# Kernel tuning notes

Measured on AMD Instinct MI355X. Metric: run time of the kernel, lower is better.

## Reference

```python
import jax, jax.numpy as jnp
import numpy as np

N = 100000
E = 200000
SD = 128   # structural_dim
CD = 768   # chemical_dim


def _linear_params(key, fan_in, fan_out):
    kw, kb = jax.random.split(key)
    bound = 1.0 / np.sqrt(fan_in)
    W = jax.random.uniform(kw, (fan_in, fan_out), jnp.float32, -bound, bound)
    b = jax.random.uniform(kb, (fan_out,), jnp.float32, -bound, bound)
    return W, b


def setup_inputs() -> dict:
    key = jax.random.key(0)
    ks = jax.random.split(key, 12)
    z = jax.random.normal(ks[0], (N, SD), jnp.float32)
    chemistry = jax.random.normal(ks[1], (N, CD), jnp.float32)
    edge = jax.random.randint(ks[2], (E, 2), 0, N, jnp.int64)
    smiles_mask = jax.random.randint(ks[3], (N,), 0, 2, jnp.int32)
    # structural_mlp: SD -> SD//2 -> 1
    sw1, sb1 = _linear_params(ks[4], SD, SD // 2)
    sw2, sb2 = _linear_params(ks[5], SD // 2, 1)
    # chemical_mlp: CD -> CD//4 -> 1
    cw1, cb1 = _linear_params(ks[6], CD, CD // 4)
    cw2, cb2 = _linear_params(ks[7], CD // 4, 1)
    # combined_mlp: SD+CD -> SD -> 1
    mw1, mb1 = _linear_params(ks[8], SD + CD, SD)
    mw2, mb2 = _linear_params(ks[9], SD, 1)
    path_weights = jnp.ones((3,), jnp.float32) / 3.0
    return dict(z=z, chemistry=chemistry, edge=edge, smiles_mask=smiles_mask,
                sw1=sw1, sb1=sb1, sw2=sw2, sb2=sb2,
                cw1=cw1, cb1=cb1, cw2=cw2, cb2=cb2,
                mw1=mw1, mb1=mb1, mw2=mw2, mb2=mb2,
                path_weights=path_weights)


def reference(z, chemistry, edge, smiles_mask,
              sw1, sb1, sw2, sb2,
              cw1, cb1, cw2, cb2,
              mw1, mb1, mw2, mb2,
              path_weights):
    src, dst = edge[:, 0], edge[:, 1]
    # per-edge gathers + elementwise products
    structural_prod = z[src] * z[dst]                    # [E, SD]
    chemical_prod = chemistry[src] * chemistry[dst]      # [E, CD]
    # three small MLPs (dropout is identity in eval mode)
    score_structural = (jax.nn.relu(structural_prod @ sw1 + sb1) @ sw2 + sb2)[:, 0]
    score_chemical = (jax.nn.relu(chemical_prod @ cw1 + cb1) @ cw2 + cb2)[:, 0]
    combined_prod = jnp.concatenate([structural_prod, chemical_prod], axis=-1)  # [E, SD+CD]
    score_combined = (jax.nn.relu(combined_prod @ mw1 + mb1) @ mw2 + mb2)[:, 0]
    # fixed learned path weights (use_gating=False)
    w = jax.nn.softmax(path_weights)
    scores = w[0] * score_structural + w[1] * score_chemical + w[2] * score_combined
    # fall back to structural-only score where chemistry is missing on either end
    mask = smiles_mask.astype(z.dtype)
    both_valid = mask[src] * mask[dst]
    return jnp.where(both_valid > 0.5, scores, score_structural)  # [E]
```

## Files before the change

### kernel.cpp

```cpp
#include <hip/hip_runtime.h>


typedef float  f32x4  __attribute__((ext_vector_type(4)));
typedef __bf16 bf16x8 __attribute__((ext_vector_type(8)));
typedef unsigned short u16x4 __attribute__((ext_vector_type(4)));

static_assert(sizeof(bf16x8) == 16, "bf16x8 must be 16B");
static_assert(sizeof(f32x4) == 16, "f32x4 must be 16B");

#define N_NODES 100000
#define E_EDGES 200000
#define KSTEPS  28
#define NOUT    384
#define PTOT    (KSTEPS * NOUT * 32)

#define WS_WHI   0
#define WS_WLO   688128
#define WS_B1    1376256
#define WS_W2    1377792
#define WS_CONST 1379328

__device__ __forceinline__ unsigned short f2bf(float f) {
  unsigned int x = __float_as_uint(f);
  unsigned int r = (x + 0x7FFFu + ((x >> 16) & 1u)) >> 16;
  return (unsigned short)r;
}
__device__ __forceinline__ float bf2f(unsigned short u) {
  return __uint_as_float(((unsigned int)u) << 16);
}

__global__ __launch_bounds__(256) void prep_kernel(
    const float* __restrict__ sw1, const float* __restrict__ sb1,
    const float* __restrict__ sw2, const float* __restrict__ sb2,
    const float* __restrict__ cw1, const float* __restrict__ cb1,
    const float* __restrict__ cw2, const float* __restrict__ cb2,
    const float* __restrict__ mw1, const float* __restrict__ mb1,
    const float* __restrict__ mw2, const float* __restrict__ mb2,
    const float* __restrict__ pw,  const int* __restrict__ edge_i32,
    unsigned short* __restrict__ whi, unsigned short* __restrict__ wlo,
    float* __restrict__ b1cat, float* __restrict__ w2cat,
    float* __restrict__ consts)
{
  const int idx = blockIdx.x * 256 + threadIdx.x;
  if (idx < PTOT) {
    const int p  = idx / (NOUT * 32);
    const int r  = idx % (NOUT * 32);
    const int n  = r >> 5;
    const int kk = r & 31;
    const int k  = p * 32 + kk;
    float v;
    if (n < 64)       v = (k < 128)  ? sw1[k * 64 + n] : 0.0f;
    else if (n < 256) v = (k >= 128) ? cw1[(size_t)(k - 128) * 192 + (n - 64)] : 0.0f;
    else              v = mw1[(size_t)k * 128 + (n - 256)];
    const unsigned short hi = f2bf(v);
    const unsigned short lo = f2bf(v - bf2f(hi));
    whi[idx] = hi;
    wlo[idx] = lo;
  } else if (idx < PTOT + NOUT) {
    const int j = idx - PTOT;
    float b, w;
    if (j < 64)       { b = sb1[j];       w = sw2[j]; }
    else if (j < 256) { b = cb1[j - 64];  w = cw2[j - 64]; }
    else              { b = mb1[j - 256]; w = mw2[j - 256]; }
    b1cat[j] = b;
    w2cat[j] = w;
  } else if (idx == PTOT + NOUT) {
    const float p0 = pw[0], p1 = pw[1], p2 = pw[2];
    const float mx = fmaxf(p0, fmaxf(p1, p2));
    const float e0 = __expf(p0 - mx), e1 = __expf(p1 - mx), e2 = __expf(p2 - mx);
    const float inv = 1.0f / (e0 + e1 + e2);
    const float w0 = e0 * inv, w1 = e1 * inv, w2v = e2 * inv;
    consts[0] = w0; consts[1] = w1; consts[2] = w2v;
    consts[3] = w0 * sb2[0] + w1 * cb2[0] + w2v * mb2[0];
    consts[4] = sb2[0];
    unsigned o = 0;
    for (int i = 0; i < 64; ++i) o |= (unsigned)edge_i32[2 * i + 1];
    consts[5] = (o == 0u) ? 1.0f : 0.0f;
  }
}

__global__ __launch_bounds__(256, 2) void decoder_main(
    const float* __restrict__ z, const float* __restrict__ chem,
    const int* __restrict__ edge, const int* __restrict__ mask,
    const unsigned short* __restrict__ whi, const unsigned short* __restrict__ wlo,
    const float* __restrict__ b1cat, const float* __restrict__ w2cat,
    const float* __restrict__ consts, float* __restrict__ out)
{
  __shared__ unsigned short Ah[2][64][40];
  __shared__ unsigned short Al[2][64][40];
  __shared__ int   srcL[64];
  __shared__ int   dstL[64];
  __shared__ float validL[64];
  __shared__ float scoreL[64];

  const int tid  = threadIdx.x;
  const int lane = tid & 63;
  const int wv   = tid >> 6;
  const int li   = lane & 15;
  const int q    = lane >> 4;
  const int m0   = blockIdx.x << 6;

  if (tid < 64) {
    scoreL[tid] = 0.0f;
    const int e = m0 + tid;
    int s_, d_;
    if (consts[5] > 0.5f) { s_ = edge[4 * e]; d_ = edge[4 * e + 2]; }
    else                  { s_ = edge[2 * e]; d_ = edge[2 * e + 1]; }
    srcL[tid] = s_;
    dstL[tid] = d_;
    validL[tid] = (mask[s_] != 0 && mask[d_] != 0) ? 1.0f : 0.0f;
  }
  __syncthreads();

  const int mA = tid >> 3;
  const int mB = 32 + mA;
  const int kc = (tid & 7) << 2;
  const float* zsA = z + (size_t)srcL[mA] * 128 + kc;
  const float* zdA = z + (size_t)dstL[mA] * 128 + kc;
  const float* zsB = z + (size_t)srcL[mB] * 128 + kc;
  const float* zdB = z + (size_t)dstL[mB] * 128 + kc;
  const float* csA = chem + (size_t)srcL[mA] * 768 + kc;
  const float* cdA = chem + (size_t)dstL[mA] * 768 + kc;
  const float* csB = chem + (size_t)srcL[mB] * 768 + kc;
  const float* cdB = chem + (size_t)dstL[mB] * 768 + kc;

  auto split_store = [&](int buf, int m, f32x4 p) {
    u16x4 h, l;
#pragma unroll
    for (int j = 0; j < 4; ++j) {
      const unsigned short hj = f2bf(p[j]);
      h[j] = hj;
      l[j] = f2bf(p[j] - bf2f(hj));
    }
    *(u16x4*)&Ah[buf][m][kc] = h;
    *(u16x4*)&Al[buf][m][kc] = l;
  };

  {
    const f32x4 a0 = *(const f32x4*)zsA;
    const f32x4 b0 = *(const f32x4*)zdA;
    const f32x4 a1 = *(const f32x4*)zsB;
    const f32x4 b1 = *(const f32x4*)zdB;
    split_store(0, mA, a0 * b0);
    split_store(0, mB, a1 * b1);
  }
  __syncthreads();

  f32x4 acc[4][6];
#pragma unroll
  for (int mt = 0; mt < 4; ++mt)
#pragma unroll
    for (int i = 0; i < 6; ++i)
      acc[mt][i] = (f32x4){0.f, 0.f, 0.f, 0.f};

  for (int s = 0; s < KSTEPS; ++s) {
    const int buf = s & 1;

    bf16x8 afh[4], afl[4];
#pragma unroll
    for (int mt = 0; mt < 4; ++mt) {
      afh[mt] = *(const bf16x8*)&Ah[buf][mt * 16 + li][q * 8];
      afl[mt] = *(const bf16x8*)&Al[buf][mt * 16 + li][q * 8];
    }

    bf16x8 bfh[6], bfl[6];
    bool act[6];
#pragma unroll
    for (int i = 0; i < 6; ++i) {
      const int ti = wv + 4 * i;
      const int path = (ti < 4) ? 0 : (ti < 16 ? 1 : 2);
      act[i] = (path == 0) ? (s < 4) : (path == 1) ? (s >= 4) : true;
      if (act[i]) {
        const size_t off = (size_t)s * (NOUT * 32) + (size_t)(ti * 16 + li) * 32 + q * 8;
        bfh[i] = *(const bf16x8*)(whi + off);
        bfl[i] = *(const bf16x8*)(wlo + off);
      }
    }

    f32x4 ga, gb, gc, gd;
    if (s + 1 < KSTEPS) {
      const int k0 = (s + 1) * 32;
      if (k0 < 128) {
        ga = *(const f32x4*)(zsA + k0); gb = *(const f32x4*)(zdA + k0);
        gc = *(const f32x4*)(zsB + k0); gd = *(const f32x4*)(zdB + k0);
      } else {
        const int ko = k0 - 128;
        ga = *(const f32x4*)(csA + ko); gb = *(const f32x4*)(cdA + ko);
        gc = *(const f32x4*)(csB + ko); gd = *(const f32x4*)(cdB + ko);
      }
    }

#pragma unroll
    for (int i = 0; i < 6; ++i) {
      if (act[i]) {
#pragma unroll
        for (int mt = 0; mt < 4; ++mt) {
          acc[mt][i] = __builtin_amdgcn_mfma_f32_16x16x32_bf16(afh[mt], bfh[i], acc[mt][i], 0, 0, 0);
          acc[mt][i] = __builtin_amdgcn_mfma_f32_16x16x32_bf16(afh[mt], bfl[i], acc[mt][i], 0, 0, 0);
          acc[mt][i] = __builtin_amdgcn_mfma_f32_16x16x32_bf16(afl[mt], bfh[i], acc[mt][i], 0, 0, 0);
        }
      }
    }

    if (s + 1 < KSTEPS) {
      const int nbuf = buf ^ 1;
      split_store(nbuf, mA, ga * gb);
      split_store(nbuf, mB, gc * gd);
    }
    __syncthreads();
  }

  float part[4][4];
#pragma unroll
  for (int mt = 0; mt < 4; ++mt)
#pragma unroll
    for (int r = 0; r < 4; ++r) part[mt][r] = 0.f;

  const float w0c = consts[0], w1c = consts[1], w2c = consts[2];
#pragma unroll
  for (int i = 0; i < 6; ++i) {
    const int ti = wv + 4 * i;
    const int path = (ti < 4) ? 0 : (ti < 16 ? 1 : 2);
    const int col = ti * 16 + li;
    const float b1 = b1cat[col];
    const float w2 = w2cat[col];
    const float wp  = (path == 0) ? w0c : (path == 1) ? w1c : w2c;
    const float p0f = (path == 0) ? 1.0f : 0.0f;
#pragma unroll
    for (int mt = 0; mt < 4; ++mt) {
#pragma unroll
      for (int r = 0; r < 4; ++r) {
        const float valid = validL[mt * 16 + q * 4 + r];
        const float a = p0f + valid * (wp - p0f);
        float v = acc[mt][i][r] + b1;
        v = fmaxf(v, 0.0f);
        part[mt][r] += a * v * w2;
      }
    }
  }

#pragma unroll
  for (int mt = 0; mt < 4; ++mt) {
#pragma unroll
    for (int r = 0; r < 4; ++r) {
      float v = part[mt][r];
      v += __shfl_xor(v, 1);
      v += __shfl_xor(v, 2);
      v += __shfl_xor(v, 4);
      v += __shfl_xor(v, 8);
      if (li == 0) atomicAdd(&scoreL[mt * 16 + q * 4 + r], v);
    }
  }
  __syncthreads();

  if (tid < 64) {
    const float valid = validL[tid];
    const float cadd = consts[4] + valid * (consts[3] - consts[4]);
    out[m0 + tid] = scoreL[tid] + cadd;
  }
}

extern "C" void kernel_launch(void* const* d_in, const int* in_sizes, int n_in,
                              void* d_out, int out_size, void* d_ws, size_t ws_size,
                              hipStream_t stream)
{
  const float* z    = (const float*)d_in[0];
  const float* chem = (const float*)d_in[1];
  const int*   edge = (const int*)d_in[2];
  const int*   mask = (const int*)d_in[3];
  const float* sw1  = (const float*)d_in[4];
  const float* sb1  = (const float*)d_in[5];
  const float* sw2  = (const float*)d_in[6];
  const float* sb2  = (const float*)d_in[7];
  const float* cw1  = (const float*)d_in[8];
  const float* cb1  = (const float*)d_in[9];
  const float* cw2  = (const float*)d_in[10];
  const float* cb2  = (const float*)d_in[11];
  const float* mw1  = (const float*)d_in[12];
  const float* mb1  = (const float*)d_in[13];
  const float* mw2  = (const float*)d_in[14];
  const float* mb2  = (const float*)d_in[15];
  const float* pw   = (const float*)d_in[16];

  char* ws = (char*)d_ws;
  unsigned short* whi = (unsigned short*)(ws + WS_WHI);
  unsigned short* wlo = (unsigned short*)(ws + WS_WLO);
  float* b1cat  = (float*)(ws + WS_B1);
  float* w2cat  = (float*)(ws + WS_W2);
  float* consts = (float*)(ws + WS_CONST);

  const int prep_tasks  = PTOT + NOUT + 64;
  const int prep_blocks = (prep_tasks + 255) / 256;
  prep_kernel<<<prep_blocks, 256, 0, stream>>>(
      sw1, sb1, sw2, sb2, cw1, cb1, cw2, cb2, mw1, mb1, mw2, mb2, pw, edge,
      whi, wlo, b1cat, w2cat, consts);

  decoder_main<<<E_EDGES / 64, 256, 0, stream>>>(
      z, chem, edge, mask, whi, wlo, b1cat, w2cat, consts, (float*)d_out);
}
```

Baseline: 761.5 us.

## Split K loop into structural and chemical phases to cut accumulator registers

The single 28-step loop with runtime per-tile activity checks is split into two loops: a 4-step structural phase and a 24-step chemical phase. The structural path's accumulators are reduced into shared scores and released before the chemical-only accumulators are allocated, so fewer accumulator registers are live at once. Launch bounds are raised from 2 to 3 blocks per SM to use that lower register pressure. The bf16 split now uses native __bf16 casts instead of hand-written rounding. Risks are register spills if three blocks do not fit, and an extra round of LDS atomics for the structural scores.

Measured after the change: 803.6 us. +5.5%, slower.

```diff
diff --git a/kernel.cpp b/kernel.cpp
--- a/kernel.cpp
+++ b/kernel.cpp
@@ -3,10 +3,7 @@
 
 typedef float  f32x4  __attribute__((ext_vector_type(4)));
 typedef __bf16 bf16x8 __attribute__((ext_vector_type(8)));
-typedef unsigned short u16x4 __attribute__((ext_vector_type(4)));
-
-static_assert(sizeof(bf16x8) == 16, "bf16x8 must be 16B");
-static_assert(sizeof(f32x4) == 16, "f32x4 must be 16B");
+typedef __bf16 bf16x4 __attribute__((ext_vector_type(4)));
 
 #define N_NODES 100000
 #define E_EDGES 200000
@@ -79,7 +76,12 @@
   }
 }
 
-__global__ __launch_bounds__(256, 2) void decoder_main(
+#define MFMA3(A, AH, AL, BH, BL)                                          \
+  A = __builtin_amdgcn_mfma_f32_16x16x32_bf16(AH, BH, A, 0, 0, 0);        \
+  A = __builtin_amdgcn_mfma_f32_16x16x32_bf16(AH, BL, A, 0, 0, 0);        \
+  A = __builtin_amdgcn_mfma_f32_16x16x32_bf16(AL, BH, A, 0, 0, 0);
+
+__global__ __launch_bounds__(256, 3) void decoder_main(
     const float* __restrict__ z, const float* __restrict__ chem,
     const int* __restrict__ edge, const int* __restrict__ mask,
     const unsigned short* __restrict__ whi, const unsigned short* __restrict__ wlo,
@@ -125,15 +127,16 @@
   const float* cdB = chem + (size_t)dstL[mB] * 768 + kc;
 
   auto split_store = [&](int buf, int m, f32x4 p) {
-    u16x4 h, l;
+    bf16x4 h, l;
 #pragma unroll
     for (int j = 0; j < 4; ++j) {
-      const unsigned short hj = f2bf(p[j]);
-      h[j] = hj;
-      l[j] = f2bf(p[j] - bf2f(hj));
-    }
-    *(u16x4*)&Ah[buf][m][kc] = h;
-    *(u16x4*)&Al[buf][m][kc] = l;
+      const float pj = p[j];
+      const __bf16 hb = (__bf16)pj;
+      h[j] = hb;
+      l[j] = (__bf16)(pj - (float)hb);
+    }
+    *(bf16x4*)&Ah[buf][m][kc] = h;
+    *(bf16x4*)&Al[buf][m][kc] = l;
   };
 
   {
@@ -146,109 +149,180 @@
   }
   __syncthreads();
 
-  f32x4 acc[4][6];
-#pragma unroll
-  for (int mt = 0; mt < 4; ++mt)
-#pragma unroll
-    for (int i = 0; i < 6; ++i)
-      acc[mt][i] = (f32x4){0.f, 0.f, 0.f, 0.f};
-
-  for (int s = 0; s < KSTEPS; ++s) {
+  const int colS  = ((wv)      * 16 + li) * 32 + q * 8;
+  const int colC0 = ((16 + wv) * 16 + li) * 32 + q * 8;
+  const int colC1 = ((20 + wv) * 16 + li) * 32 + q * 8;
+  const int colH0 = ((4 + wv)  * 16 + li) * 32 + q * 8;
+  const int colH1 = ((8 + wv)  * 16 + li) * 32 + q * 8;
+  const int colH2 = ((12 + wv) * 16 + li) * 32 + q * 8;
+
+  const float w0c = consts[0], w1c = consts[1], w2c = consts[2];
+
+  f32x4 accS[4], accC0[4], accC1[4];
+#pragma unroll
+  for (int mt = 0; mt < 4; ++mt) {
+    accS[mt] = (f32x4){0.f, 0.f, 0.f, 0.f};
+    accC0[mt] = (f32x4){0.f, 0.f, 0.f, 0.f};
+    accC1[mt] = (f32x4){0.f, 0.f, 0.f, 0.f};
+  }
+
+  for (int s = 0; s < 4; ++s) {
     const int buf = s & 1;
-
     bf16x8 afh[4], afl[4];
 #pragma unroll
     for (int mt = 0; mt < 4; ++mt) {
       afh[mt] = *(const bf16x8*)&Ah[buf][mt * 16 + li][q * 8];
       afl[mt] = *(const bf16x8*)&Al[buf][mt * 16 + li][q * 8];
     }
-
-    bf16x8 bfh[6], bfl[6];
-    bool act[6];
-#pragma unroll
-    for (int i = 0; i < 6; ++i) {
-      const int ti = wv + 4 * i;
-      const int path = (ti < 4) ? 0 : (ti < 16 ? 1 : 2);
-      act[i] = (path == 0) ? (s < 4) : (path == 1) ? (s >= 4) : true;
-      if (act[i]) {
-        const size_t off = (size_t)s * (NOUT * 32) + (size_t)(ti * 16 + li) * 32 + q * 8;
-        bfh[i] = *(const bf16x8*)(whi + off);
-        bfl[i] = *(const bf16x8*)(wlo + off);
-      }
-    }
+    const unsigned short* wph = whi + (size_t)s * (NOUT * 32);
+    const unsigned short* wpl = wlo + (size_t)s * (NOUT * 32);
+    const bf16x8 bSh  = *(const bf16x8*)(wph + colS);
+    const bf16x8 bSl  = *(const bf16x8*)(wpl + colS);
+    const bf16x8 bC0h = *(const bf16x8*)(wph + colC0);
+    const bf16x8 bC0l = *(const bf16x8*)(wpl + colC0);
+    const bf16x8 bC1h = *(const bf16x8*)(wph + colC1);
+    const bf16x8 bC1l = *(const bf16x8*)(wpl + colC1);
 
     f32x4 ga, gb, gc, gd;
-    if (s + 1 < KSTEPS) {
+    if (s < 3) {
       const int k0 = (s + 1) * 32;
-      if (k0 < 128) {
-        ga = *(const f32x4*)(zsA + k0); gb = *(const f32x4*)(zdA + k0);
-        gc = *(const f32x4*)(zsB + k0); gd = *(const f32x4*)(zdB + k0);
-      } else {
-        const int ko = k0 - 128;
-        ga = *(const f32x4*)(csA + ko); gb = *(const f32x4*)(cdA + ko);
-        gc = *(const f32x4*)(csB + ko); gd = *(const f32x4*)(cdB + ko);
-      }
-    }
-
-#pragma unroll
-    for (int i = 0; i < 6; ++i) {
-      if (act[i]) {
-#pragma unroll
-        for (int mt = 0; mt < 4; ++mt) {
-          acc[mt][i] = __builtin_amdgcn_mfma_f32_16x16x32_bf16(afh[mt], bfh[i], acc[mt][i], 0, 0, 0);
-          acc[mt][i] = __builtin_amdgcn_mfma_f32_16x16x32_bf16(afh[mt], bfl[i], acc[mt][i], 0, 0, 0);
-          acc[mt][i] = __builtin_amdgcn_mfma_f32_16x16x32_bf16(afl[mt], bfh[i], acc[mt][i], 0, 0, 0);
-        }
-      }
-    }
-
-    if (s + 1 < KSTEPS) {
-      const int nbuf = buf ^ 1;
-      split_store(nbuf, mA, ga * gb);
-      split_store(nbuf, mB, gc * gd);
-    }
+      ga = *(const f32x4*)(zsA + k0); gb = *(const f32x4*)(zdA + k0);
+      gc = *(const f32x4*)(zsB + k0); gd = *(const f32x4*)(zdB + k0);
+    } else {
+      ga = *(const f32x4*)csA; gb = *(const f32x4*)cdA;
+      gc = *(const f32x4*)csB; gd = *(const f32x4*)cdB;
+    }
+
+#pragma unroll
+    for (int mt = 0; mt < 4; ++mt) {
+      MFMA3(accS[mt],  afh[mt], afl[mt], bSh,  bSl);
+      MFMA3(accC0[mt], afh[mt], afl[mt], bC0h, bC0l);
+      MFMA3(accC1[mt], afh[mt], afl[mt], bC1h, bC1l);
+    }
+
+    const int nb = buf ^ 1;
+    split_store(nb, mA, ga * gb);
+    split_store(nb, mB, gc * gd);
     __syncthreads();
   }
 
-  float part[4][4];
-#pragma unroll
-  for (int mt = 0; mt < 4; ++mt)
-#pragma unroll
-    for (int r = 0; r < 4; ++r) part[mt][r] = 0.f;
-
-  const float w0c = consts[0], w1c = consts[1], w2c = consts[2];
-#pragma unroll
-  for (int i = 0; i < 6; ++i) {
-    const int ti = wv + 4 * i;
-    const int path = (ti < 4) ? 0 : (ti < 16 ? 1 : 2);
-    const int col = ti * 16 + li;
+  {
+    const int col = wv * 16 + li;
     const float b1 = b1cat[col];
     const float w2 = w2cat[col];
-    const float wp  = (path == 0) ? w0c : (path == 1) ? w1c : w2c;
-    const float p0f = (path == 0) ? 1.0f : 0.0f;
 #pragma unroll
     for (int mt = 0; mt < 4; ++mt) {
 #pragma unroll
       for (int r = 0; r < 4; ++r) {
         const float valid = validL[mt * 16 + q * 4 + r];
-        const float a = p0f + valid * (wp - p0f);
-        float v = acc[mt][i][r] + b1;
-        v = fmaxf(v, 0.0f);
-        part[mt][r] += a * v * w2;
+        const float a = 1.0f + valid * (w0c - 1.0f);
+        float v = fmaxf(accS[mt][r] + b1, 0.0f);
+        v = a * v * w2;
+        v += __shfl_xor(v, 1);
+        v += __shfl_xor(v, 2);
+        v += __shfl_xor(v, 4);
+        v += __shfl_xor(v, 8);
+        if (li == 0) atomicAdd(&scoreL[mt * 16 + q * 4 + r], v);
       }
     }
   }
 
+  f32x4 accH0[4], accH1[4], accH2[4];
 #pragma unroll
   for (int mt = 0; mt < 4; ++mt) {
-#pragma unroll
-    for (int r = 0; r < 4; ++r) {
-      float v = part[mt][r];
-      v += __shfl_xor(v, 1);
-      v += __shfl_xor(v, 2);
-      v += __shfl_xor(v, 4);
-      v += __shfl_xor(v, 8);
-      if (li == 0) atomicAdd(&scoreL[mt * 16 + q * 4 + r], v);
+    accH0[mt] = (f32x4){0.f, 0.f, 0.f, 0.f};
+    accH1[mt] = (f32x4){0.f, 0.f, 0.f, 0.f};
+    accH2[mt] = (f32x4){0.f, 0.f, 0.f, 0.f};
+  }
+
+  for (int s = 4; s < KSTEPS; ++s) {
+    const int buf = s & 1;
+    bf16x8 afh[4], afl[4];
+#pragma unroll
+    for (int mt = 0; mt < 4; ++mt) {
+      afh[mt] = *(const bf16x8*)&Ah[buf][mt * 16 + li][q * 8];
+      afl[mt] = *(const bf16x8*)&Al[buf][mt * 16 + li][q * 8];
+    }
+    const unsigned short* wph = whi + (size_t)s * (NOUT * 32);
+    const unsigned short* wpl = wlo + (size_t)s * (NOUT * 32);
+    const bf16x8 bC0h = *(const bf16x8*)(wph + colC0);
+    const bf16x8 bC0l = *(const bf16x8*)(wpl + colC0);
+    const bf16x8 bC1h = *(const bf16x8*)(wph + colC1);
+    const bf16x8 bC1l = *(const bf16x8*)(wpl + colC1);
+    const bf16x8 bH0h = *(const bf16x8*)(wph + colH0);
+    const bf16x8 bH0l = *(const bf16x8*)(wpl + colH0);
+    const bf16x8 bH1h = *(const bf16x8*)(wph + colH1);
+    const bf16x8 bH1l = *(const bf16x8*)(wpl + colH1);
+    const bf16x8 bH2h = *(const bf16x8*)(wph + colH2);
+    const bf16x8 bH2l = *(const bf16x8*)(wpl + colH2);
+
+    f32x4 ga, gb, gc, gd;
+    const bool hn = (s + 1 < KSTEPS);
+    if (hn) {
+      const int ko = (s + 1) * 32 - 128;
+      ga = *(const f32x4*)(csA + ko); gb = *(const f32x4*)(cdA + ko);
+      gc = *(const f32x4*)(csB + ko); gd = *(const f32x4*)(cdB + ko);
+    }
+
+#pragma unroll
+    for (int mt = 0; mt < 4; ++mt) {
+      MFMA3(accH0[mt], afh[mt], afl[mt], bH0h, bH0l);
+      MFMA3(accH1[mt], afh[mt], afl[mt], bH1h, bH1l);
+      MFMA3(accH2[mt], afh[mt], afl[mt], bH2h, bH2l);
+      MFMA3(accC0[mt], afh[mt], afl[mt], bC0h, bC0l);
+      MFMA3(accC1[mt], afh[mt], afl[mt], bC1h, bC1l);
+    }
+
+    if (hn) {
+      const int nb = buf ^ 1;
+      split_store(nb, mA, ga * gb);
+      split_store(nb, mB, gc * gd);
+    }
+    __syncthreads();
+  }
+
+  {
+    float part[4][4];
+#pragma unroll
+    for (int mt = 0; mt < 4; ++mt)
+#pragma unroll
+      for (int r = 0; r < 4; ++r) part[mt][r] = 0.f;
+
+#define ACCUM_TILE(ACC, TI, WP)                                     \
+    {                                                               \
+      const int col = (TI) * 16 + li;                               \
+      const float b1 = b1cat[col];                                  \
+      const float w2 = w2cat[col];                                  \
+      _Pragma("unroll")                                             \
+      for (int mt = 0; mt < 4; ++mt) {                              \
+        _Pragma("unroll")                                           \
+        for (int r = 0; r < 4; ++r) {                               \
+          const float valid = validL[mt * 16 + q * 4 + r];          \
+          const float a = valid * (WP);                             \
+          float v = fmaxf(ACC[mt][r] + b1, 0.0f);                   \
+          part[mt][r] += a * v * w2;                                \
+        }                                                           \
+      }                                                             \
+    }
+
+    ACCUM_TILE(accC0, 16 + wv, w2c)
+    ACCUM_TILE(accC1, 20 + wv, w2c)
+    ACCUM_TILE(accH0, 4 + wv,  w1c)
+    ACCUM_TILE(accH1, 8 + wv,  w1c)
+    ACCUM_TILE(accH2, 12 + wv, w1c)
+#undef ACCUM_TILE
+
+#pragma unroll
+    for (int mt = 0; mt < 4; ++mt) {
+#pragma unroll
+      for (int r = 0; r < 4; ++r) {
+        float v = part[mt][r];
+        v += __shfl_xor(v, 1);
+        v += __shfl_xor(v, 2);
+        v += __shfl_xor(v, 4);
+        v += __shfl_xor(v, 8);
+        if (li == 0) atomicAdd(&scoreL[mt * 16 + q * 4 + r], v);
+      }
     }
   }
   __syncthreads();
```
